# Kernel tuning notes

Hardware: AMD Instinct MI355X
Metric: run time of the kernel (lower is better)

## Reference

```python
import jax, jax.numpy as jnp
import numpy as np

N_ITEMS = 100000
N_USERS = 16384
HIST = 50
TEXT_DIM = 256
GCN_DIM = 128
HIDDEN_DIM = 512
TOWER_DIM = 128


def _l2norm(x, eps=1e-12):
    # F.normalize(dim=1): x / max(||x||, eps)
    n = jnp.sqrt(jnp.sum(x * x, axis=1, keepdims=True))
    return x / jnp.maximum(n, eps)


def setup_inputs() -> dict:
    key = jax.random.key(0)
    ks = jax.random.split(key, 10)
    s1i = 1.0 / np.sqrt(TEXT_DIM + GCN_DIM)
    s2i = 1.0 / np.sqrt(HIDDEN_DIM)
    s1u = 1.0 / np.sqrt(GCN_DIM + TOWER_DIM)
    return {
        "item_text_emb": jax.random.normal(ks[0], (N_ITEMS, TEXT_DIM), jnp.float32),
        "gcn_item_emb": jax.random.normal(ks[1], (N_ITEMS, GCN_DIM), jnp.float32),
        "gcn_user_emb": jax.random.normal(ks[2], (N_USERS, GCN_DIM), jnp.float32),
        "hist_idx": jax.random.randint(ks[3], (N_USERS, HIST), 0, N_ITEMS),
        "W1i": jax.random.normal(ks[4], (TEXT_DIM + GCN_DIM, HIDDEN_DIM), jnp.float32) * s1i,
        "b1i": jnp.zeros((HIDDEN_DIM,), jnp.float32),
        "W2i": jax.random.normal(ks[5], (HIDDEN_DIM, TOWER_DIM), jnp.float32) * s2i,
        "b2i": jnp.zeros((TOWER_DIM,), jnp.float32),
        "W1u": jax.random.normal(ks[6], (GCN_DIM + TOWER_DIM, HIDDEN_DIM), jnp.float32) * s1u,
        "b1u": jnp.zeros((HIDDEN_DIM,), jnp.float32),
        "W2u": jax.random.normal(ks[7], (HIDDEN_DIM, TOWER_DIM), jnp.float32) * s2i,
        "b2u": jnp.zeros((TOWER_DIM,), jnp.float32),
    }


def reference(item_text_emb, gcn_item_emb, gcn_user_emb, hist_idx,
              W1i, b1i, W2i, b2i, W1u, b1u, W2u, b2u):
    # encode_items: MLP over concat(text, gcn) features, then L2 normalize
    item_feat = jnp.concatenate([item_text_emb, gcn_item_emb], axis=1)  # [N_items, text+gcn]
    h = jax.nn.relu(item_feat @ W1i + b1i)
    item_emb = _l2norm(h @ W2i + b2i)  # [N_items, TOWER_DIM]
    # encode_users: per-user gather of history item embeddings + mean pooling
    hist = jnp.mean(item_emb[hist_idx], axis=1)  # [N_users, TOWER_DIM]
    fused = jnp.concatenate([gcn_user_emb, hist], axis=1)
    hu = jax.nn.relu(fused @ W1u + b1u)
    user_emb = _l2norm(hu @ W2u + b2u)  # [N_users, TOWER_DIM]
    return user_emb
```

## Files before the change

### kernel.cpp

```cpp
#include <hip/hip_runtime.h>
#include <hip/hip_bf16.h>

#define HIST 50
#define N_ITEMS 100000
#define N_USERS 16384

typedef __bf16 bf8 __attribute__((ext_vector_type(8)));
typedef float  f4  __attribute__((ext_vector_type(4)));

__device__ __forceinline__ unsigned short f2bf(float x) {
    unsigned u = __builtin_bit_cast(unsigned, x);
    u += 0x7fffu + ((u >> 16) & 1u);
    return (unsigned short)(u >> 16);
}
__device__ __forceinline__ float bf2f(unsigned b) {
    unsigned u = b << 16;
    return __builtin_bit_cast(float, u);
}

__global__ void pack_weights(const float* __restrict__ W1i, const float* __restrict__ W2i,
                             const float* __restrict__ W1u, const float* __restrict__ W2u,
                             unsigned short* __restrict__ dstbase)
{
    int i = blockIdx.x * 256 + threadIdx.x;
    const float* W; unsigned short* dst; int N, KS, loc;
    if (i < 24576)      { W = W1i; dst = dstbase;          N = 512; KS = 12; loc = i; }
    else if (i < 32768) { W = W2i; dst = dstbase + 196608; N = 128; KS = 16; loc = i - 24576; }
    else if (i < 49152) { W = W1u; dst = dstbase + 262144; N = 512; KS = 8;  loc = i - 32768; }
    else                { W = W2u; dst = dstbase + 393216; N = 128; KS = 16; loc = i - 49152; }
    int l = loc & 63, fi = loc >> 6;
    int ks = fi % KS, nt = fi / KS;
    int q = l >> 4, c = l & 15;
    const float* src = W + (size_t)(ks * 32 + q * 8) * N + nt * 16 + c;
    unsigned o[4];
    #pragma unroll
    for (int k = 0; k < 4; ++k) {
        unsigned lo = f2bf(src[(2 * k) * N]);
        unsigned hi = f2bf(src[(2 * k + 1) * N]);
        o[k] = lo | (hi << 16);
    }
    uint4 v; v.x = o[0]; v.y = o[1]; v.z = o[2]; v.w = o[3];
    ((uint4*)dst)[(size_t)(nt * KS + ks) * 64 + l] = v;
}

template<int KS1, int ASTR, bool OUT_BF16>
__device__ __forceinline__ void tower_core(
    unsigned short* U, const float* b1s, const float* b2s, float* sumsq,
    const bf8* __restrict__ w1f, const bf8* __restrict__ w2f,
    void* __restrict__ outp, int row0, int nval, int tid)
{
    const int HSTR = 520;
    const int l = tid & 63, w = tid >> 6;
    const int q = l >> 4, c = l & 15;

    f4 acc1[4][4];
    #pragma unroll
    for (int i = 0; i < 4; ++i)
        #pragma unroll
        for (int j = 0; j < 4; ++j) acc1[i][j] = (f4)0.0f;

    const unsigned short* ap = U + c * ASTR + q * 8;
    #pragma unroll
    for (int ks = 0; ks < KS1; ++ks) {
        bf8 a[4], b[4];
        #pragma unroll
        for (int rt = 0; rt < 4; ++rt)
            a[rt] = *(const bf8*)(ap + rt * 16 * ASTR + ks * 32);
        #pragma unroll
        for (int nt = 0; nt < 4; ++nt)
            b[nt] = w1f[(size_t)((w * 4 + nt) * KS1 + ks) * 64 + l];
        #pragma unroll
        for (int rt = 0; rt < 4; ++rt)
            #pragma unroll
            for (int nt = 0; nt < 4; ++nt)
                acc1[rt][nt] = __builtin_amdgcn_mfma_f32_16x16x32_bf16(a[rt], b[nt], acc1[rt][nt], 0, 0, 0);
    }
    __syncthreads();

    #pragma unroll
    for (int nt = 0; nt < 4; ++nt) {
        int col = w * 64 + nt * 16 + c;
        float bias = b1s[col];
        #pragma unroll
        for (int rt = 0; rt < 4; ++rt)
            #pragma unroll
            for (int reg = 0; reg < 4; ++reg) {
                float h = fmaxf(acc1[rt][nt][reg] + bias, 0.0f);
                U[(rt * 16 + q * 4 + reg) * HSTR + col] = f2bf(h);
            }
    }
    __syncthreads();

    const int rg = w >> 2, jj = w & 3;
    f4 acc2[2][2];
    #pragma unroll
    for (int i = 0; i < 2; ++i)
        #pragma unroll
        for (int j = 0; j < 2; ++j) acc2[i][j] = (f4)0.0f;

    const unsigned short* hp = U + (size_t)(rg * 32 + c) * HSTR + q * 8;
    #pragma unroll
    for (int ks = 0; ks < 16; ++ks) {
        bf8 a[2], b[2];
        #pragma unroll
        for (int i = 0; i < 2; ++i)
            a[i] = *(const bf8*)(hp + i * 16 * HSTR + ks * 32);
        #pragma unroll
        for (int j = 0; j < 2; ++j)
            b[j] = w2f[(size_t)((jj * 2 + j) * 16 + ks) * 64 + l];
        #pragma unroll
        for (int i = 0; i < 2; ++i)
            #pragma unroll
            for (int j = 0; j < 2; ++j)
                acc2[i][j] = __builtin_amdgcn_mfma_f32_16x16x32_bf16(a[i], b[j], acc2[i][j], 0, 0, 0);
    }

    float v[2][2][4];
    #pragma unroll
    for (int i = 0; i < 2; ++i)
        #pragma unroll
        for (int j = 0; j < 2; ++j) {
            float bias = b2s[jj * 32 + j * 16 + c];
            #pragma unroll
            for (int reg = 0; reg < 4; ++reg)
                v[i][j][reg] = acc2[i][j][reg] + bias;
        }
    #pragma unroll
    for (int i = 0; i < 2; ++i)
        #pragma unroll
        for (int reg = 0; reg < 4; ++reg) {
            float s = v[i][0][reg] * v[i][0][reg] + v[i][1][reg] * v[i][1][reg];
            s += __shfl_xor(s, 1); s += __shfl_xor(s, 2);
            s += __shfl_xor(s, 4); s += __shfl_xor(s, 8);
            if (c == 0) atomicAdd(&sumsq[rg * 32 + i * 16 + q * 4 + reg], s);
        }
    __syncthreads();
    #pragma unroll
    for (int i = 0; i < 2; ++i)
        #pragma unroll
        for (int reg = 0; reg < 4; ++reg) {
            int row = rg * 32 + i * 16 + q * 4 + reg;
            if (row < nval) {
                float inv = 1.0f / fmaxf(sqrtf(sumsq[row]), 1e-12f);
                #pragma unroll
                for (int j = 0; j < 2; ++j) {
                    int col = jj * 32 + j * 16 + c;
                    float o = v[i][j][reg] * inv;
                    if (OUT_BF16)
                        ((unsigned short*)outp)[(size_t)(row0 + row) * 128 + col] = f2bf(o);
                    else
                        ((float*)outp)[(size_t)(row0 + row) * 128 + col] = o;
                }
            }
        }
}

#define ASI 392
#define ASU 264

__global__ __launch_bounds__(512, 4) void item_kernel(
    const float* __restrict__ text, const float* __restrict__ gcn,
    const bf8* __restrict__ w1f, const float* __restrict__ b1,
    const bf8* __restrict__ w2f, const float* __restrict__ b2,
    unsigned short* __restrict__ item_bf)
{
    __shared__ __align__(16) unsigned short U[64 * 520];
    __shared__ float b1s[512], b2s[128], sumsq[64];
    const int tid = threadIdx.x;
    const int row0 = blockIdx.x * 64;
    const int nval = min(64, N_ITEMS - row0);
    const float4* t4 = (const float4*)text;
    const float4* g4 = (const float4*)gcn;
    #pragma unroll
    for (int j = 0; j < 8; ++j) {
        int idx = tid + j * 512; int r = idx >> 6, c4 = idx & 63;
        float4 x = (r < nval) ? t4[(size_t)(row0 + r) * 64 + c4] : make_float4(0.f,0.f,0.f,0.f);
        ushort4 s; s.x = f2bf(x.x); s.y = f2bf(x.y); s.z = f2bf(x.z); s.w = f2bf(x.w);
        *(ushort4*)(U + r * ASI + c4 * 4) = s;
    }
    #pragma unroll
    for (int j = 0; j < 4; ++j) {
        int idx = tid + j * 512; int r = idx >> 5, c4 = idx & 31;
        float4 x = (r < nval) ? g4[(size_t)(row0 + r) * 32 + c4] : make_float4(0.f,0.f,0.f,0.f);
        ushort4 s; s.x = f2bf(x.x); s.y = f2bf(x.y); s.z = f2bf(x.z); s.w = f2bf(x.w);
        *(ushort4*)(U + r * ASI + 256 + c4 * 4) = s;
    }
    b1s[tid] = b1[tid];
    if (tid < 128) b2s[tid] = b2[tid];
    if (tid < 64)  sumsq[tid] = 0.0f;
    __syncthreads();
    tower_core<12, ASI, true>(U, b1s, b2s, sumsq, w1f, w2f, item_bf, row0, nval, tid);
}

__global__ __launch_bounds__(512, 4) void user_kernel(
    const float* __restrict__ gcnu, const int* __restrict__ hist,
    const unsigned short* __restrict__ item_bf,
    const bf8* __restrict__ w1f, const float* __restrict__ b1,
    const bf8* __restrict__ w2f, const float* __restrict__ b2,
    float* __restrict__ outp)
{
    __shared__ __align__(16) unsigned short U[64 * 520];
    __shared__ float b1s[512], b2s[128], sumsq[64];
    const int tid = threadIdx.x;
    const int u0 = blockIdx.x * 64;
    const float4* g4 = (const float4*)gcnu;
    #pragma unroll
    for (int j = 0; j < 4; ++j) {
        int idx = tid + j * 512; int r = idx >> 5, c4 = idx & 31;
        float4 x = g4[(size_t)(u0 + r) * 32 + c4];
        ushort4 s; s.x = f2bf(x.x); s.y = f2bf(x.y); s.z = f2bf(x.z); s.w = f2bf(x.w);
        *(ushort4*)(U + r * ASU + c4 * 4) = s;
    }
    b1s[tid] = b1[tid];
    if (tid < 128) b2s[tid] = b2[tid];
    if (tid < 64)  sumsq[tid] = 0.0f;
    {
        const int u = tid >> 3, g = tid & 7;
        float f[16];
        #pragma unroll
        for (int k = 0; k < 16; ++k) f[k] = 0.0f;
        const int* hrow = hist + (size_t)(u0 + u) * HIST;
        #pragma unroll 5
        for (int t = 0; t < HIST; ++t) {
            int id = hrow[t];
            const uint4* p = (const uint4*)(item_bf + (size_t)id * 128 + g * 16);
            #pragma unroll
            for (int h = 0; h < 2; ++h) {
                uint4 x = p[h];
                unsigned vs[4] = {x.x, x.y, x.z, x.w};
                #pragma unroll
                for (int k = 0; k < 4; ++k) {
                    f[h * 8 + 2 * k]     += bf2f(vs[k] & 0xffffu);
                    f[h * 8 + 2 * k + 1] += bf2f(vs[k] >> 16);
                }
            }
        }
        unsigned o[8];
        #pragma unroll
        for (int k = 0; k < 8; ++k)
            o[k] = (unsigned)f2bf(f[2 * k] * 0.02f) | ((unsigned)f2bf(f[2 * k + 1] * 0.02f) << 16);
        unsigned short* dstp = U + u * ASU + 128 + g * 16;
        #pragma unroll
        for (int h = 0; h < 2; ++h) {
            uint4 s; s.x = o[h*4]; s.y = o[h*4+1]; s.z = o[h*4+2]; s.w = o[h*4+3];
            *(uint4*)(dstp + h * 8) = s;
        }
    }
    __syncthreads();
    tower_core<8, ASU, false>(U, b1s, b2s, sumsq, w1f, w2f, outp, u0, 64, tid);
}

extern "C" void kernel_launch(void* const* d_in, const int* in_sizes, int n_in,
                              void* d_out, int out_size, void* d_ws, size_t ws_size,
                              hipStream_t stream) {
    const float* text = (const float*)d_in[0];
    const float* gcni = (const float*)d_in[1];
    const float* gcnu = (const float*)d_in[2];
    const int*   hist = (const int*)d_in[3];
    const float* W1i  = (const float*)d_in[4];
    const float* b1i  = (const float*)d_in[5];
    const float* W2i  = (const float*)d_in[6];
    const float* b2i  = (const float*)d_in[7];
    const float* W1u  = (const float*)d_in[8];
    const float* b1u  = (const float*)d_in[9];
    const float* W2u  = (const float*)d_in[10];
    const float* b2u  = (const float*)d_in[11];
    float* out = (float*)d_out;

    unsigned short* itemb = (unsigned short*)d_ws;
    unsigned short* pw = itemb + 12800000;

    pack_weights<<<224, 256, 0, stream>>>(W1i, W2i, W1u, W2u, pw);
    item_kernel<<<(N_ITEMS + 63) / 64, 512, 0, stream>>>(
        text, gcni, (const bf8*)pw, b1i, (const bf8*)(pw + 196608), b2i, itemb);
    user_kernel<<<N_USERS / 64, 512, 0, stream>>>(
        gcnu, hist, itemb, (const bf8*)(pw + 262144), b1u, (const bf8*)(pw + 393216), b2u, out);
}
```

Measured before the change: 320.9 us.

## Halve rows per block to 32 for higher occupancy in tower kernels

```diff
diff --git a/kernel.cpp b/kernel.cpp
--- a/kernel.cpp
+++ b/kernel.cpp
@@ -47,33 +47,29 @@
 __device__ __forceinline__ void tower_core(
     unsigned short* U, const float* b1s, const float* b2s, float* sumsq,
     const bf8* __restrict__ w1f, const bf8* __restrict__ w2f,
-    void* __restrict__ outp, int row0, int nval, int tid)
+    void* __restrict__ outp, int row0, int tid)
 {
     const int HSTR = 520;
     const int l = tid & 63, w = tid >> 6;
     const int q = l >> 4, c = l & 15;
 
-    f4 acc1[4][4];
-    #pragma unroll
-    for (int i = 0; i < 4; ++i)
+    f4 acc1[2][4];
+    #pragma unroll
+    for (int i = 0; i < 2; ++i)
         #pragma unroll
         for (int j = 0; j < 4; ++j) acc1[i][j] = (f4)0.0f;
 
     const unsigned short* ap = U + c * ASTR + q * 8;
     #pragma unroll
     for (int ks = 0; ks < KS1; ++ks) {
-        bf8 a[4], b[4];
-        #pragma unroll
-        for (int rt = 0; rt < 4; ++rt)
-            a[rt] = *(const bf8*)(ap + rt * 16 * ASTR + ks * 32);
-        #pragma unroll
-        for (int nt = 0; nt < 4; ++nt)
-            b[nt] = w1f[(size_t)((w * 4 + nt) * KS1 + ks) * 64 + l];
-        #pragma unroll
-        for (int rt = 0; rt < 4; ++rt)
-            #pragma unroll
-            for (int nt = 0; nt < 4; ++nt)
-                acc1[rt][nt] = __builtin_amdgcn_mfma_f32_16x16x32_bf16(a[rt], b[nt], acc1[rt][nt], 0, 0, 0);
+        bf8 a0 = *(const bf8*)(ap + ks * 32);
+        bf8 a1 = *(const bf8*)(ap + 16 * ASTR + ks * 32);
+        #pragma unroll
+        for (int nt = 0; nt < 4; ++nt) {
+            bf8 b = w1f[(size_t)((w * 4 + nt) * KS1 + ks) * 64 + l];
+            acc1[0][nt] = __builtin_amdgcn_mfma_f32_16x16x32_bf16(a0, b, acc1[0][nt], 0, 0, 0);
+            acc1[1][nt] = __builtin_amdgcn_mfma_f32_16x16x32_bf16(a1, b, acc1[1][nt], 0, 0, 0);
+        }
     }
     __syncthreads();
 
@@ -82,7 +78,7 @@
         int col = w * 64 + nt * 16 + c;
         float bias = b1s[col];
         #pragma unroll
-        for (int rt = 0; rt < 4; ++rt)
+        for (int rt = 0; rt < 2; ++rt)
             #pragma unroll
             for (int reg = 0; reg < 4; ++reg) {
                 float h = fmaxf(acc1[rt][nt][reg] + bias, 0.0f);
@@ -92,162 +88,139 @@
     __syncthreads();
 
     const int rg = w >> 2, jj = w & 3;
-    f4 acc2[2][2];
-    #pragma unroll
-    for (int i = 0; i < 2; ++i)
-        #pragma unroll
-        for (int j = 0; j < 2; ++j) acc2[i][j] = (f4)0.0f;
-
-    const unsigned short* hp = U + (size_t)(rg * 32 + c) * HSTR + q * 8;
+    f4 acc2[2];
+    acc2[0] = (f4)0.0f; acc2[1] = (f4)0.0f;
+
+    const unsigned short* hp = U + (size_t)(rg * 16 + c) * HSTR + q * 8;
     #pragma unroll
     for (int ks = 0; ks < 16; ++ks) {
-        bf8 a[2], b[2];
-        #pragma unroll
-        for (int i = 0; i < 2; ++i)
-            a[i] = *(const bf8*)(hp + i * 16 * HSTR + ks * 32);
-        #pragma unroll
-        for (int j = 0; j < 2; ++j)
-            b[j] = w2f[(size_t)((jj * 2 + j) * 16 + ks) * 64 + l];
-        #pragma unroll
-        for (int i = 0; i < 2; ++i)
-            #pragma unroll
-            for (int j = 0; j < 2; ++j)
-                acc2[i][j] = __builtin_amdgcn_mfma_f32_16x16x32_bf16(a[i], b[j], acc2[i][j], 0, 0, 0);
-    }
-
-    float v[2][2][4];
-    #pragma unroll
-    for (int i = 0; i < 2; ++i)
+        bf8 a = *(const bf8*)(hp + ks * 32);
+        bf8 b0 = w2f[(size_t)((jj * 2 + 0) * 16 + ks) * 64 + l];
+        bf8 b1 = w2f[(size_t)((jj * 2 + 1) * 16 + ks) * 64 + l];
+        acc2[0] = __builtin_amdgcn_mfma_f32_16x16x32_bf16(a, b0, acc2[0], 0, 0, 0);
+        acc2[1] = __builtin_amdgcn_mfma_f32_16x16x32_bf16(a, b1, acc2[1], 0, 0, 0);
+    }
+
+    float v[2][4];
+    #pragma unroll
+    for (int j = 0; j < 2; ++j) {
+        float bias = b2s[jj * 32 + j * 16 + c];
+        #pragma unroll
+        for (int reg = 0; reg < 4; ++reg)
+            v[j][reg] = acc2[j][reg] + bias;
+    }
+    #pragma unroll
+    for (int reg = 0; reg < 4; ++reg) {
+        float s = v[0][reg] * v[0][reg] + v[1][reg] * v[1][reg];
+        s += __shfl_xor(s, 1); s += __shfl_xor(s, 2);
+        s += __shfl_xor(s, 4); s += __shfl_xor(s, 8);
+        if (c == 0) atomicAdd(&sumsq[rg * 16 + q * 4 + reg], s);
+    }
+    __syncthreads();
+    #pragma unroll
+    for (int reg = 0; reg < 4; ++reg) {
+        int row = rg * 16 + q * 4 + reg;
+        float inv = 1.0f / fmaxf(sqrtf(sumsq[row]), 1e-12f);
         #pragma unroll
         for (int j = 0; j < 2; ++j) {
-            float bias = b2s[jj * 32 + j * 16 + c];
-            #pragma unroll
-            for (int reg = 0; reg < 4; ++reg)
-                v[i][j][reg] = acc2[i][j][reg] + bias;
+            int col = jj * 32 + j * 16 + c;
+            float o = v[j][reg] * inv;
+            if (OUT_BF16)
+                ((unsigned short*)outp)[(size_t)(row0 + row) * 128 + col] = f2bf(o);
+            else
+                ((float*)outp)[(size_t)(row0 + row) * 128 + col] = o;
         }
-    #pragma unroll
-    for (int i = 0; i < 2; ++i)
-        #pragma unroll
-        for (int reg = 0; reg < 4; ++reg) {
-            float s = v[i][0][reg] * v[i][0][reg] + v[i][1][reg] * v[i][1][reg];
-            s += __shfl_xor(s, 1); s += __shfl_xor(s, 2);
-            s += __shfl_xor(s, 4); s += __shfl_xor(s, 8);
-            if (c == 0) atomicAdd(&sumsq[rg * 32 + i * 16 + q * 4 + reg], s);
-        }
-    __syncthreads();
-    #pragma unroll
-    for (int i = 0; i < 2; ++i)
-        #pragma unroll
-        for (int reg = 0; reg < 4; ++reg) {
-            int row = rg * 32 + i * 16 + q * 4 + reg;
-            if (row < nval) {
-                float inv = 1.0f / fmaxf(sqrtf(sumsq[row]), 1e-12f);
-                #pragma unroll
-                for (int j = 0; j < 2; ++j) {
-                    int col = jj * 32 + j * 16 + c;
-                    float o = v[i][j][reg] * inv;
-                    if (OUT_BF16)
-                        ((unsigned short*)outp)[(size_t)(row0 + row) * 128 + col] = f2bf(o);
-                    else
-                        ((float*)outp)[(size_t)(row0 + row) * 128 + col] = o;
-                }
-            }
-        }
+    }
 }
 
 #define ASI 392
 #define ASU 264
 
-__global__ __launch_bounds__(512, 4) void item_kernel(
+__global__ __launch_bounds__(512, 8) void item_kernel(
     const float* __restrict__ text, const float* __restrict__ gcn,
     const bf8* __restrict__ w1f, const float* __restrict__ b1,
     const bf8* __restrict__ w2f, const float* __restrict__ b2,
     unsigned short* __restrict__ item_bf)
 {
-    __shared__ __align__(16) unsigned short U[64 * 520];
-    __shared__ float b1s[512], b2s[128], sumsq[64];
+    __shared__ __align__(16) unsigned short U[32 * 520];
+    __shared__ float b1s[512], b2s[128], sumsq[32];
     const int tid = threadIdx.x;
-    const int row0 = blockIdx.x * 64;
-    const int nval = min(64, N_ITEMS - row0);
+    const int row0 = blockIdx.x * 32;
     const float4* t4 = (const float4*)text;
     const float4* g4 = (const float4*)gcn;
     #pragma unroll
-    for (int j = 0; j < 8; ++j) {
+    for (int j = 0; j < 4; ++j) {
         int idx = tid + j * 512; int r = idx >> 6, c4 = idx & 63;
-        float4 x = (r < nval) ? t4[(size_t)(row0 + r) * 64 + c4] : make_float4(0.f,0.f,0.f,0.f);
+        float4 x = t4[(size_t)(row0 + r) * 64 + c4];
         ushort4 s; s.x = f2bf(x.x); s.y = f2bf(x.y); s.z = f2bf(x.z); s.w = f2bf(x.w);
         *(ushort4*)(U + r * ASI + c4 * 4) = s;
     }
     #pragma unroll
-    for (int j = 0; j < 4; ++j) {
+    for (int j = 0; j < 2; ++j) {
         int idx = tid + j * 512; int r = idx >> 5, c4 = idx & 31;
-        float4 x = (r < nval) ? g4[(size_t)(row0 + r) * 32 + c4] : make_float4(0.f,0.f,0.f,0.f);
+        float4 x = g4[(size_t)(row0 + r) * 32 + c4];
         ushort4 s; s.x = f2bf(x.x); s.y = f2bf(x.y); s.z = f2bf(x.z); s.w = f2bf(x.w);
         *(ushort4*)(U + r * ASI + 256 + c4 * 4) = s;
     }
     b1s[tid] = b1[tid];
     if (tid < 128) b2s[tid] = b2[tid];
-    if (tid < 64)  sumsq[tid] = 0.0f;
-    __syncthreads();
-    tower_core<12, ASI, true>(U, b1s, b2s, sumsq, w1f, w2f, item_bf, row0, nval, tid);
-}
-
-__global__ __launch_bounds__(512, 4) void user_kernel(
+    if (tid < 32)  sumsq[tid] = 0.0f;
+    __syncthreads();
+    tower_core<12, ASI, true>(U, b1s, b2s, sumsq, w1f, w2f, item_bf, row0, tid);
+}
+
+__global__ __launch_bounds__(512, 8) void user_kernel(
     const float* __restrict__ gcnu, const int* __restrict__ hist,
     const unsigned short* __restrict__ item_bf,
     const bf8* __restrict__ w1f, const float* __restrict__ b1,
     const bf8* __restrict__ w2f, const float* __restrict__ b2,
     float* __restrict__ outp)
 {
-    __shared__ __align__(16) unsigned short U[64 * 520];
-    __shared__ float b1s[512], b2s[128], sumsq[64];
+    __shared__ __align__(16) unsigned short U[32 * 520];
+    __shared__ float b1s[512], b2s[128], sumsq[32];
     const int tid = threadIdx.x;
-    const int u0 = blockIdx.x * 64;
+    const int u0 = blockIdx.x * 32;
+    int* hist_s = (int*)(U + 32 * ASU);
     const float4* g4 = (const float4*)gcnu;
     #pragma unroll
-    for (int j = 0; j < 4; ++j) {
+    for (int j = 0; j < 2; ++j) {
         int idx = tid + j * 512; int r = idx >> 5, c4 = idx & 31;
         float4 x = g4[(size_t)(u0 + r) * 32 + c4];
         ushort4 s; s.x = f2bf(x.x); s.y = f2bf(x.y); s.z = f2bf(x.z); s.w = f2bf(x.w);
         *(ushort4*)(U + r * ASU + c4 * 4) = s;
     }
+    for (int k = tid; k < 32 * HIST; k += 512)
+        hist_s[k] = hist[(size_t)u0 * HIST + k];
     b1s[tid] = b1[tid];
     if (tid < 128) b2s[tid] = b2[tid];
-    if (tid < 64)  sumsq[tid] = 0.0f;
+    if (tid < 32)  sumsq[tid] = 0.0f;
+    __syncthreads();
     {
-        const int u = tid >> 3, g = tid & 7;
-        float f[16];
-        #pragma unroll
-        for (int k = 0; k < 16; ++k) f[k] = 0.0f;
-        const int* hrow = hist + (size_t)(u0 + u) * HIST;
-        #pragma unroll 5
+        const int u = tid >> 4, g = tid & 15;
+        float f[8];
+        #pragma unroll
+        for (int k = 0; k < 8; ++k) f[k] = 0.0f;
+        const int* hrow = hist_s + u * HIST;
+        #pragma unroll 10
         for (int t = 0; t < HIST; ++t) {
             int id = hrow[t];
-            const uint4* p = (const uint4*)(item_bf + (size_t)id * 128 + g * 16);
+            uint4 x = *(const uint4*)(item_bf + (size_t)id * 128 + g * 8);
+            unsigned vs[4] = {x.x, x.y, x.z, x.w};
             #pragma unroll
-            for (int h = 0; h < 2; ++h) {
-                uint4 x = p[h];
-                unsigned vs[4] = {x.x, x.y, x.z, x.w};
-                #pragma unroll
-                for (int k = 0; k < 4; ++k) {
-                    f[h * 8 + 2 * k]     += bf2f(vs[k] & 0xffffu);
-                    f[h * 8 + 2 * k + 1] += bf2f(vs[k] >> 16);
-                }
+            for (int k = 0; k < 4; ++k) {
+                f[2 * k]     += bf2f(vs[k] & 0xffffu);
+                f[2 * k + 1] += bf2f(vs[k] >> 16);
             }
         }
-        unsigned o[8];
-        #pragma unroll
-        for (int k = 0; k < 8; ++k)
+        unsigned o[4];
+        #pragma unroll
+        for (int k = 0; k < 4; ++k)
             o[k] = (unsigned)f2bf(f[2 * k] * 0.02f) | ((unsigned)f2bf(f[2 * k + 1] * 0.02f) << 16);
-        unsigned short* dstp = U + u * ASU + 128 + g * 16;
-        #pragma unroll
-        for (int h = 0; h < 2; ++h) {
-            uint4 s; s.x = o[h*4]; s.y = o[h*4+1]; s.z = o[h*4+2]; s.w = o[h*4+3];
-            *(uint4*)(dstp + h * 8) = s;
-        }
-    }
-    __syncthreads();
-    tower_core<8, ASU, false>(U, b1s, b2s, sumsq, w1f, w2f, outp, u0, 64, tid);
+        uint4 s; s.x = o[0]; s.y = o[1]; s.z = o[2]; s.w = o[3];
+        *(uint4*)(U + u * ASU + 128 + g * 8) = s;
+    }
+    __syncthreads();
+    tower_core<8, ASU, false>(U, b1s, b2s, sumsq, w1f, w2f, outp, u0, tid);
 }
 
 extern "C" void kernel_launch(void* const* d_in, const int* in_sizes, int n_in,
@@ -271,8 +244,8 @@
     unsigned short* pw = itemb + 12800000;
 
     pack_weights<<<224, 256, 0, stream>>>(W1i, W2i, W1u, W2u, pw);
-    item_kernel<<<(N_ITEMS + 63) / 64, 512, 0, stream>>>(
+    item_kernel<<<N_ITEMS / 32, 512, 0, stream>>>(
         text, gcni, (const bf8*)pw, b1i, (const bf8*)(pw + 196608), b2i, itemb);
-    user_kernel<<<N_USERS / 64, 512, 0, stream>>>(
+    user_kernel<<<N_USERS / 32, 512, 0, stream>>>(
         gcnu, hist, itemb, (const bf8*)(pw + 262144), b1u, (const bf8*)(pw + 393216), b2u, out);
 }
```

Result: no change. 320.3 us (-0.2%).
